# Kernel tuning notes

Hardware: AMD Instinct MI355X
Metric: run time of the kernel (lower is better)

## Reference

```python
import jax, jax.numpy as jnp
import numpy as np

P_THRESH = 20  # p=0.2 * 100
# direction -> (di, dj): masked pixel (i,j) writes input[i,j] to x[i+di, j+dj], then avg to x[i,j]
OFFSETS = {0: (-1, -1), 1: (-1, 0), 2: (-1, 1), 3: (0, -1), 4: (0, 0), 5: (0, 1), 6: (1, -1), 7: (1, 0)}


def _shift(a, di, dj):
    """out[i+di, j+dj] = a[i, j] on last two axes; out-of-range -> 0/False."""
    H, W = a.shape[-2], a.shape[-1]
    pad = [(0, 0)] * (a.ndim - 2) + [(max(di, 0), max(-di, 0)), (max(dj, 0), max(-dj, 0))]
    p = jnp.pad(a, pad)
    sh, sw = max(-di, 0), max(-dj, 0)
    return p[..., sh:sh + H, sw:sw + W]


def _avg3x3_reflect(x):
    H, W = x.shape[-2], x.shape[-1]
    p = jnp.pad(x, [(0, 0), (0, 0), (1, 1), (1, 1)], mode='reflect')
    s = jnp.zeros_like(x)
    for i in range(3):
        for j in range(3):
            s = s + p[..., i:i + H, j:j + W]
    return s / 9.0


def brown_forward(input, dir, prob):
    avg = _avg3x3_reflect(input)
    pos = prob <= P_THRESH
    x = input
    for d in range(8):  # sequential, matching torch in-place write order
        di, dj = OFFSETS[d]
        m = (dir == d) & pos
        if d == 4:
            x = jnp.where(m, avg, x)  # mm: only avg write
        else:
            sm = _shift(m, di, dj)                       # neighbor-target mask
            x = jnp.where(sm, _shift(input, di, dj), x)  # x[i+di,j+dj] = input[i,j]
            mv = _shift(sm, -di, -dj)                    # mask restricted to valid region
            x = jnp.where(mv, avg, x)                    # x[i,j] = avg[i,j]
    return x


def setup_inputs() -> dict:
    key = jax.random.key(0)
    k1, k2, k3 = jax.random.split(key, 3)
    shape = (32, 64, 128, 128)
    return {
        'input': jax.random.normal(k1, shape, dtype=jnp.float32),
        'dir': jax.random.randint(k2, shape, 0, 8, dtype=jnp.int32),
        'prob': jax.random.randint(k3, shape, 1, 100, dtype=jnp.int32),
    }


def reference(input, dir, prob):
    return brown_forward(input, dir, prob)
```

## Files before the change

### kernel.cpp

```cpp
#include <hip/hip_runtime.h>
#include <cstddef>

#define H 128
#define W 128
#define WROWS 8
#define LROWS 10
#define P_THRESH 20

typedef float nf4 __attribute__((ext_vector_type(4)));
typedef __attribute__((address_space(1))) const unsigned int glo_u32;
typedef __attribute__((address_space(3))) unsigned int lds_u32;

__global__ __launch_bounds__(256, 6)
void brown_kernel(const float* __restrict__ inp,
                  const int*  __restrict__ dirp,
                  const int*  __restrict__ prb,
                  float* __restrict__ out)
{
    __shared__ __align__(16) float s_in[4 * LROWS * W];
    __shared__ unsigned int        s_mk[4 * LROWS * 32];

    const int tid   = threadIdx.x;
    const int wid   = tid >> 6;
    const int lane  = tid & 63;
    const int bid   = blockIdx.x;
    const int slice = bid >> 2;
    const int r0    = (bid & 3) << 5;
    const int wr0   = r0 + wid * WROWS;
    const size_t base = (size_t)slice * (size_t)(H * W);

    float*        s_in_w = s_in + wid * (LROWS * W);
    unsigned int* s_mk_w = s_mk + wid * (LROWS * 32);

    int4 dvv[5], pvv[5];
    #pragma unroll
    for (int w = 0; w < 5; ++w) {
        const int idx = w * 64 + lane;
        const int L   = idx >> 5;
        const int c4  = idx & 31;
        const int gr  = wr0 - 1 + L;
        if ((unsigned)gr < (unsigned)H) {
            dvv[w] = ((const int4*)(dirp + base + (size_t)gr * W))[c4];
            pvv[w] = ((const int4*)(prb  + base + (size_t)gr * W))[c4];
        } else {
            dvv[w] = make_int4(8, 8, 8, 8);
            pvv[w] = make_int4(100, 100, 100, 100);
        }
    }
    #pragma unroll
    for (int w = 0; w < 5; ++w) {
        const int idx = w * 64 + lane;
        const int L   = idx >> 5;
        const int c4  = idx & 31;
        const int gr  = wr0 - 1 + L;
        const int gri = (gr < 0) ? 1 : ((gr >= H) ? (H - 2) : gr);
        const float* gp = inp + base + (size_t)gri * W + c4 * 4;
        __builtin_amdgcn_global_load_lds((glo_u32*)gp, (lds_u32*)(s_in_w + idx * 4), 16, 0, 0);
    }
    #pragma unroll
    for (int w = 0; w < 5; ++w) {
        const int idx = w * 64 + lane;
        const unsigned a  = (pvv[w].x <= P_THRESH) ? (unsigned)dvv[w].x : 8u;
        const unsigned b  = (pvv[w].y <= P_THRESH) ? (unsigned)dvv[w].y : 8u;
        const unsigned cc = (pvv[w].z <= P_THRESH) ? (unsigned)dvv[w].z : 8u;
        const unsigned d  = (pvv[w].w <= P_THRESH) ? (unsigned)dvv[w].w : 8u;
        s_mk_w[idx] = a | (b << 8) | (cc << 16) | (d << 24);
    }
    asm volatile("s_waitcnt vmcnt(0)" ::: "memory");

    const int cq   = lane & 31;
    const int rh   = lane >> 6 ? 0 : (lane >> 5);
    const int j0   = cq << 2;
    const int lrb  = rh << 2;
    const int cqm1 = (cq > 0)  ? cq - 1 : 0;
    const int cqp1 = (cq < 31) ? cq + 1 : 31;

    auto load_row = [&](int L, float v[6], unsigned& ma, unsigned& mb) {
        const float4   c   = ((const float4*)(s_in_w + L * W))[cq];
        const unsigned mwc = s_mk_w[L * 32 + cq];
        const unsigned mwl = s_mk_w[L * 32 + cqm1];
        const unsigned mwr = s_mk_w[L * 32 + cqp1];
        const float lf = __shfl_up(c.w, 1);
        const float rt = __shfl_down(c.x, 1);
        v[1] = c.x; v[2] = c.y; v[3] = c.z; v[4] = c.w;
        v[0] = (cq > 0)  ? lf : c.y;
        v[5] = (cq < 31) ? rt : c.z;
        const unsigned ml = (cq > 0)  ? (mwl >> 24)  : 8u;
        const unsigned mr = (cq < 31) ? (mwr & 255u) : 8u;
        ma = (mwc << 8) | ml;
        mb = (mwc >> 8) | (mr << 24);
    };

    float va[6], vb[6], vc[6];
    unsigned maa, mab, mba, mbb, mca, mcb;
    load_row(lrb + 0, va, maa, mab);
    load_row(lrb + 1, vb, mba, mbb);

    #pragma unroll
    for (int rr = 0; rr < 4; ++rr) {
        load_row(lrb + rr + 2, vc, mca, mcb);

        const int gi = wr0 + (rh << 2) + rr;
        float cs[6];
        #pragma unroll
        for (int w = 0; w < 6; ++w) cs[w] = va[w] + vb[w] + vc[w];

        nf4 res;
        #pragma unroll
        for (int p = 0; p < 4; ++p) {
            const float avg = (cs[p] + cs[p + 1] + cs[p + 2]) * (1.0f / 9.0f);
            const unsigned wTop = (p < 2) ? (maa >> (8 * p)) : (mab >> (8 * (p - 2)));
            const unsigned wMid = (p < 2) ? (mba >> (8 * p)) : (mbb >> (8 * (p - 2)));
            const unsigned wBot = (p < 2) ? (mca >> (8 * p)) : (mcb >> (8 * (p - 2)));

            float val = vb[p + 1];
            int dl = -1;
            if (((wBot >> 16) & 255u) == 0u) { val = vc[p + 2]; dl = 0; }
            if (((wBot >>  8) & 255u) == 1u) { val = vc[p + 1]; dl = 1; }
            if (( wBot        & 255u) == 2u) { val = vc[p];     dl = 2; }
            if (((wMid >> 16) & 255u) == 3u) { val = vb[p + 2]; dl = 3; }
            if (( wMid        & 255u) == 5u) { val = vb[p];     dl = 5; }
            if (((wTop >> 16) & 255u) == 6u) { val = va[p + 2]; dl = 6; }
            if (((wTop >>  8) & 255u) == 7u) { val = va[p + 1]; dl = 7; }

            const int msel = (int)((wMid >> 8) & 255u);
            const int q3 = (msel * 11) >> 5;
            const int di = q3 - 1;
            const int dj = msel - q3 * 3 - 1;
            const int ti = gi + di;
            const int tj = j0 + p + dj;
            const bool bok = (msel < 8) & ((unsigned)ti < 128u) & ((unsigned)tj < 128u);
            if (bok & (msel >= dl)) val = avg;
            res[p] = val;
        }
        __builtin_nontemporal_store(res, (nf4*)(out + base + (size_t)gi * W) + cq);

        #pragma unroll
        for (int w = 0; w < 6; ++w) { va[w] = vb[w]; vb[w] = vc[w]; }
        maa = mba; mab = mbb; mba = mca; mbb = mcb;
    }
}

extern "C" void kernel_launch(void* const* d_in, const int* in_sizes, int n_in,
                              void* d_out, int out_size, void* d_ws, size_t ws_size,
                              hipStream_t stream) {
    const float* inp  = (const float*)d_in[0];
    const int*   dirp = (const int*)d_in[1];
    const int*   prb  = (const int*)d_in[2];
    float* out = (float*)d_out;

    const int slices = in_sizes[0] / (H * W);
    const int grid = slices * 4;
    brown_kernel<<<grid, 256, 0, stream>>>(inp, dirp, prb, out);
}
```

Baseline: 392.6 us.

## Process whole slice per block with double-buffered LDS prefetch pipeline

Each block now handles a full 128x128 slice in four 32-row stages instead of one stage per block. While one stage is computed, the next stage's inp tile is prefetched into a second LDS buffer and its dir/prob values into registers. The aim is to overlap global-load latency with compute inside a block. In exchange the grid shrinks fourfold, LDS per block doubles, occupancy drops (launch bounds 6 to 3), and correctness now depends on hand-counted vmcnt waits.

```diff
diff --git a/kernel.cpp b/kernel.cpp
--- a/kernel.cpp
+++ b/kernel.cpp
@@ -3,142 +3,177 @@
 
 #define H 128
 #define W 128
-#define WROWS 8
+#define P_THRESH 20
 #define LROWS 10
-#define P_THRESH 20
 
 typedef float nf4 __attribute__((ext_vector_type(4)));
 typedef __attribute__((address_space(1))) const unsigned int glo_u32;
 typedef __attribute__((address_space(3))) unsigned int lds_u32;
 
-__global__ __launch_bounds__(256, 6)
+__global__ __launch_bounds__(256, 3)
 void brown_kernel(const float* __restrict__ inp,
                   const int*  __restrict__ dirp,
                   const int*  __restrict__ prb,
                   float* __restrict__ out)
 {
-    __shared__ __align__(16) float s_in[4 * LROWS * W];
-    __shared__ unsigned int        s_mk[4 * LROWS * 32];
+    __shared__ __align__(16) float s_in[8 * LROWS * W];
+    __shared__ unsigned int        s_mk[8 * LROWS * 32];
 
-    const int tid   = threadIdx.x;
-    const int wid   = tid >> 6;
-    const int lane  = tid & 63;
-    const int bid   = blockIdx.x;
-    const int slice = bid >> 2;
-    const int r0    = (bid & 3) << 5;
-    const int wr0   = r0 + wid * WROWS;
-    const size_t base = (size_t)slice * (size_t)(H * W);
+    const int tid  = threadIdx.x;
+    const int wid  = tid >> 6;
+    const int lane = tid & 63;
+    const size_t base = (size_t)blockIdx.x * (size_t)(H * W);
 
-    float*        s_in_w = s_in + wid * (LROWS * W);
-    unsigned int* s_mk_w = s_mk + wid * (LROWS * 32);
+    float*        sb0 = s_in + (wid * 2 + 0) * (LROWS * W);
+    float*        sb1 = s_in + (wid * 2 + 1) * (LROWS * W);
+    unsigned int* sm0 = s_mk + (wid * 2 + 0) * (LROWS * 32);
+    unsigned int* sm1 = s_mk + (wid * 2 + 1) * (LROWS * 32);
 
-    int4 dvv[5], pvv[5];
-    #pragma unroll
-    for (int w = 0; w < 5; ++w) {
-        const int idx = w * 64 + lane;
-        const int L   = idx >> 5;
-        const int c4  = idx & 31;
-        const int gr  = wr0 - 1 + L;
-        if ((unsigned)gr < (unsigned)H) {
-            dvv[w] = ((const int4*)(dirp + base + (size_t)gr * W))[c4];
-            pvv[w] = ((const int4*)(prb  + base + (size_t)gr * W))[c4];
-        } else {
-            dvv[w] = make_int4(8, 8, 8, 8);
-            pvv[w] = make_int4(100, 100, 100, 100);
+    auto issue_masks = [&](int r, int4 (&dv)[5], int4 (&pv)[5]) {
+        const int wr0 = (r << 5) + (wid << 3);
+        #pragma unroll
+        for (int w = 0; w < 5; ++w) {
+            const int idx = w * 64 + lane;
+            const int Lr  = idx >> 5;
+            const int c4  = idx & 31;
+            const int gr  = wr0 - 1 + Lr;
+            if ((unsigned)gr < (unsigned)H) {
+                dv[w] = ((const int4*)(dirp + base + (size_t)gr * W))[c4];
+                pv[w] = ((const int4*)(prb  + base + (size_t)gr * W))[c4];
+            } else {
+                dv[w] = make_int4(8, 8, 8, 8);
+                pv[w] = make_int4(100, 100, 100, 100);
+            }
         }
-    }
-    #pragma unroll
-    for (int w = 0; w < 5; ++w) {
-        const int idx = w * 64 + lane;
-        const int L   = idx >> 5;
-        const int c4  = idx & 31;
-        const int gr  = wr0 - 1 + L;
-        const int gri = (gr < 0) ? 1 : ((gr >= H) ? (H - 2) : gr);
-        const float* gp = inp + base + (size_t)gri * W + c4 * 4;
-        __builtin_amdgcn_global_load_lds((glo_u32*)gp, (lds_u32*)(s_in_w + idx * 4), 16, 0, 0);
-    }
-    #pragma unroll
-    for (int w = 0; w < 5; ++w) {
-        const int idx = w * 64 + lane;
-        const unsigned a  = (pvv[w].x <= P_THRESH) ? (unsigned)dvv[w].x : 8u;
-        const unsigned b  = (pvv[w].y <= P_THRESH) ? (unsigned)dvv[w].y : 8u;
-        const unsigned cc = (pvv[w].z <= P_THRESH) ? (unsigned)dvv[w].z : 8u;
-        const unsigned d  = (pvv[w].w <= P_THRESH) ? (unsigned)dvv[w].w : 8u;
-        s_mk_w[idx] = a | (b << 8) | (cc << 16) | (d << 24);
-    }
-    asm volatile("s_waitcnt vmcnt(0)" ::: "memory");
+    };
+    auto issue_dma = [&](int r, float* sb) {
+        const int wr0 = (r << 5) + (wid << 3);
+        #pragma unroll
+        for (int w = 0; w < 5; ++w) {
+            const int idx = w * 64 + lane;
+            const int Lr  = idx >> 5;
+            const int c4  = idx & 31;
+            const int gr  = wr0 - 1 + Lr;
+            const int gri = (gr < 0) ? 1 : ((gr >= H) ? (H - 2) : gr);
+            const float* gp = inp + base + (size_t)gri * W + c4 * 4;
+            __builtin_amdgcn_global_load_lds((glo_u32*)gp, (lds_u32*)(sb + idx * 4), 16, 0, 0);
+        }
+        asm volatile("" ::: "memory");
+    };
+    auto pack_masks = [&](int4 (&dv)[5], int4 (&pv)[5], unsigned int* smk) {
+        #pragma unroll
+        for (int w = 0; w < 5; ++w) {
+            const int idx = w * 64 + lane;
+            const unsigned a  = (pv[w].x <= P_THRESH) ? (unsigned)dv[w].x : 8u;
+            const unsigned b  = (pv[w].y <= P_THRESH) ? (unsigned)dv[w].y : 8u;
+            const unsigned cc = (pv[w].z <= P_THRESH) ? (unsigned)dv[w].z : 8u;
+            const unsigned d  = (pv[w].w <= P_THRESH) ? (unsigned)dv[w].w : 8u;
+            smk[idx] = a | (b << 8) | (cc << 16) | (d << 24);
+        }
+    };
 
     const int cq   = lane & 31;
-    const int rh   = lane >> 6 ? 0 : (lane >> 5);
+    const int rh   = lane >> 5;
     const int j0   = cq << 2;
     const int lrb  = rh << 2;
     const int cqm1 = (cq > 0)  ? cq - 1 : 0;
     const int cqp1 = (cq < 31) ? cq + 1 : 31;
 
-    auto load_row = [&](int L, float v[6], unsigned& ma, unsigned& mb) {
-        const float4   c   = ((const float4*)(s_in_w + L * W))[cq];
-        const unsigned mwc = s_mk_w[L * 32 + cq];
-        const unsigned mwl = s_mk_w[L * 32 + cqm1];
-        const unsigned mwr = s_mk_w[L * 32 + cqp1];
-        const float lf = __shfl_up(c.w, 1);
-        const float rt = __shfl_down(c.x, 1);
-        v[1] = c.x; v[2] = c.y; v[3] = c.z; v[4] = c.w;
-        v[0] = (cq > 0)  ? lf : c.y;
-        v[5] = (cq < 31) ? rt : c.z;
-        const unsigned ml = (cq > 0)  ? (mwl >> 24)  : 8u;
-        const unsigned mr = (cq < 31) ? (mwr & 255u) : 8u;
-        ma = (mwc << 8) | ml;
-        mb = (mwc >> 8) | (mr << 24);
+    auto compute = [&](int r, const float* sb, const unsigned int* smk) {
+        const int wr0 = (r << 5) + (wid << 3);
+
+        auto load_row = [&](int L, float v[6], unsigned& ma, unsigned& mb) {
+            const float4   c   = ((const float4*)(sb + L * W))[cq];
+            const unsigned mwc = smk[L * 32 + cq];
+            const unsigned mwl = smk[L * 32 + cqm1];
+            const unsigned mwr = smk[L * 32 + cqp1];
+            const float lf = __shfl_up(c.w, 1);
+            const float rt = __shfl_down(c.x, 1);
+            v[1] = c.x; v[2] = c.y; v[3] = c.z; v[4] = c.w;
+            v[0] = (cq > 0)  ? lf : c.y;
+            v[5] = (cq < 31) ? rt : c.z;
+            const unsigned ml = (cq > 0)  ? (mwl >> 24)  : 8u;
+            const unsigned mr = (cq < 31) ? (mwr & 255u) : 8u;
+            ma = (mwc << 8) | ml;
+            mb = (mwc >> 8) | (mr << 24);
+        };
+
+        float va[6], vb[6], vc[6];
+        unsigned maa, mab, mba, mbb, mca, mcb;
+        load_row(lrb + 0, va, maa, mab);
+        load_row(lrb + 1, vb, mba, mbb);
+
+        #pragma unroll
+        for (int rr = 0; rr < 4; ++rr) {
+            load_row(lrb + rr + 2, vc, mca, mcb);
+
+            const int gi = wr0 + lrb + rr;
+            float cs[6];
+            #pragma unroll
+            for (int w = 0; w < 6; ++w) cs[w] = va[w] + vb[w] + vc[w];
+
+            nf4 res;
+            #pragma unroll
+            for (int p = 0; p < 4; ++p) {
+                const float avg = (cs[p] + cs[p + 1] + cs[p + 2]) * (1.0f / 9.0f);
+                const unsigned wTop = (p < 2) ? (maa >> (8 * p)) : (mab >> (8 * (p - 2)));
+                const unsigned wMid = (p < 2) ? (mba >> (8 * p)) : (mbb >> (8 * (p - 2)));
+                const unsigned wBot = (p < 2) ? (mca >> (8 * p)) : (mcb >> (8 * (p - 2)));
+
+                float val = vb[p + 1];
+                int dl = -1;
+                if (((wBot >> 16) & 255u) == 0u) { val = vc[p + 2]; dl = 0; }
+                if (((wBot >>  8) & 255u) == 1u) { val = vc[p + 1]; dl = 1; }
+                if (( wBot        & 255u) == 2u) { val = vc[p];     dl = 2; }
+                if (((wMid >> 16) & 255u) == 3u) { val = vb[p + 2]; dl = 3; }
+                if (( wMid        & 255u) == 5u) { val = vb[p];     dl = 5; }
+                if (((wTop >> 16) & 255u) == 6u) { val = va[p + 2]; dl = 6; }
+                if (((wTop >>  8) & 255u) == 7u) { val = va[p + 1]; dl = 7; }
+
+                const int msel = (int)((wMid >> 8) & 255u);
+                const int q3 = (msel * 11) >> 5;
+                const int di = q3 - 1;
+                const int dj = msel - q3 * 3 - 1;
+                const int ti = gi + di;
+                const int tj = j0 + p + dj;
+                const bool bok = (msel < 8) & ((unsigned)ti < 128u) & ((unsigned)tj < 128u);
+                if (bok & (msel >= dl)) val = avg;
+                res[p] = val;
+            }
+            __builtin_nontemporal_store(res, (nf4*)(out + base + (size_t)gi * W) + cq);
+
+            #pragma unroll
+            for (int w = 0; w < 6; ++w) { va[w] = vb[w]; vb[w] = vc[w]; }
+            maa = mba; mab = mbb; mba = mca; mbb = mcb;
+        }
     };
 
-    float va[6], vb[6], vc[6];
-    unsigned maa, mab, mba, mbb, mca, mcb;
-    load_row(lrb + 0, va, maa, mab);
-    load_row(lrb + 1, vb, mba, mbb);
+    int4 dv0[5], pv0[5], dv1[5], pv1[5];
 
-    #pragma unroll
-    for (int rr = 0; rr < 4; ++rr) {
-        load_row(lrb + rr + 2, vc, mca, mcb);
+    issue_masks(0, dv0, pv0);
+    issue_dma(0, sb0);
 
-        const int gi = wr0 + (rh << 2) + rr;
-        float cs[6];
-        #pragma unroll
-        for (int w = 0; w < 6; ++w) cs[w] = va[w] + vb[w] + vc[w];
+    issue_masks(1, dv1, pv1);
+    issue_dma(1, sb1);
+    pack_masks(dv0, pv0, sm0);
+    asm volatile("s_waitcnt vmcnt(15)" ::: "memory");
+    compute(0, sb0, sm0);
 
-        nf4 res;
-        #pragma unroll
-        for (int p = 0; p < 4; ++p) {
-            const float avg = (cs[p] + cs[p + 1] + cs[p + 2]) * (1.0f / 9.0f);
-            const unsigned wTop = (p < 2) ? (maa >> (8 * p)) : (mab >> (8 * (p - 2)));
-            const unsigned wMid = (p < 2) ? (mba >> (8 * p)) : (mbb >> (8 * (p - 2)));
-            const unsigned wBot = (p < 2) ? (mca >> (8 * p)) : (mcb >> (8 * (p - 2)));
+    issue_masks(2, dv0, pv0);
+    issue_dma(2, sb0);
+    pack_masks(dv1, pv1, sm1);
+    asm volatile("s_waitcnt vmcnt(19)" ::: "memory");
+    compute(1, sb1, sm1);
 
-            float val = vb[p + 1];
-            int dl = -1;
-            if (((wBot >> 16) & 255u) == 0u) { val = vc[p + 2]; dl = 0; }
-            if (((wBot >>  8) & 255u) == 1u) { val = vc[p + 1]; dl = 1; }
-            if (( wBot        & 255u) == 2u) { val = vc[p];     dl = 2; }
-            if (((wMid >> 16) & 255u) == 3u) { val = vb[p + 2]; dl = 3; }
-            if (( wMid        & 255u) == 5u) { val = vb[p];     dl = 5; }
-            if (((wTop >> 16) & 255u) == 6u) { val = va[p + 2]; dl = 6; }
-            if (((wTop >>  8) & 255u) == 7u) { val = va[p + 1]; dl = 7; }
+    issue_masks(3, dv1, pv1);
+    issue_dma(3, sb1);
+    pack_masks(dv0, pv0, sm0);
+    asm volatile("s_waitcnt vmcnt(19)" ::: "memory");
+    compute(2, sb0, sm0);
 
-            const int msel = (int)((wMid >> 8) & 255u);
-            const int q3 = (msel * 11) >> 5;
-            const int di = q3 - 1;
-            const int dj = msel - q3 * 3 - 1;
-            const int ti = gi + di;
-            const int tj = j0 + p + dj;
-            const bool bok = (msel < 8) & ((unsigned)ti < 128u) & ((unsigned)tj < 128u);
-            if (bok & (msel >= dl)) val = avg;
-            res[p] = val;
-        }
-        __builtin_nontemporal_store(res, (nf4*)(out + base + (size_t)gi * W) + cq);
-
-        #pragma unroll
-        for (int w = 0; w < 6; ++w) { va[w] = vb[w]; vb[w] = vc[w]; }
-        maa = mba; mab = mbb; mba = mca; mbb = mcb;
-    }
+    pack_masks(dv1, pv1, sm1);
+    asm volatile("s_waitcnt vmcnt(4)" ::: "memory");
+    compute(3, sb1, sm1);
 }
 
 extern "C" void kernel_launch(void* const* d_in, const int* in_sizes, int n_in,
@@ -150,6 +185,5 @@
     float* out = (float*)d_out;
 
     const int slices = in_sizes[0] / (H * W);
-    const int grid = slices * 4;
-    brown_kernel<<<grid, 256, 0, stream>>>(inp, dirp, prb, out);
+    brown_kernel<<<slices, 256, 0, stream>>>(inp, dirp, prb, out);
 }
```

New measurement: 416.0 us. 1.06x slower.
